# Performance work log

Hardware: AMD Instinct MI355X
Metric: run time of the kernel (lower is better)

## Reference

```python
import jax, jax.numpy as jnp
import numpy as np

N_NODES = 50000
N_EDGES = 800000
N_GRAPHS = 64
FEAT, EMB, HID, VOCAB = 128, 256, 512, 512


def setup_inputs() -> dict:
    key = jax.random.key(0)
    ks = jax.random.split(key, 16)
    def w(k, shape, fan_in):
        return jax.random.normal(k, shape, jnp.float32) / np.sqrt(fan_in)
    return {
        "prev_symbol": jax.random.randint(ks[0], (N_GRAPHS,), 0, VOCAB, jnp.int32),
        "x": jax.random.normal(ks[1], (N_NODES, FEAT), jnp.float32),
        "edge_index": jax.random.randint(ks[2], (2, N_EDGES), 0, N_NODES, jnp.int64),
        "batch": jnp.sort(jax.random.randint(ks[3], (N_NODES,), 0, N_GRAPHS, jnp.int64)),
        "W_root1": w(ks[4], (FEAT, EMB), FEAT),
        "W_rel1": w(ks[5], (FEAT, EMB), FEAT),
        "b1": jnp.zeros((EMB,), jnp.float32),
        "W_root2": w(ks[6], (EMB, HID), EMB),
        "W_rel2": w(ks[7], (EMB, HID), EMB),
        "b2": jnp.zeros((HID,), jnp.float32),
        "Wh": w(ks[8], (HID, HID), HID),
        "bh": jnp.zeros((HID,), jnp.float32),
        "Wc": w(ks[9], (HID, HID), HID),
        "bc": jnp.zeros((HID,), jnp.float32),
        "Wout": w(ks[10], (HID, VOCAB), HID),
        "bout": jnp.zeros((VOCAB,), jnp.float32),
    }


def _rgcn(x, edge_index, W_root, W_rel, b):
    # single-relation RGCNConv: root transform + mean-aggregated neighbor messages
    src, dst = edge_index[0], edge_index[1]
    msg = x[src] @ W_rel                                   # [E, out]
    agg = jax.ops.segment_sum(msg, dst, num_segments=N_NODES)
    cnt = jax.ops.segment_sum(jnp.ones((src.shape[0],), x.dtype), dst,
                              num_segments=N_NODES)
    agg = agg / jnp.maximum(cnt, 1.0)[:, None]
    return x @ W_root + agg + b


def reference(prev_symbol, x, edge_index, batch,
              W_root1, W_rel1, b1, W_root2, W_rel2, b2,
              Wh, bh, Wc, bc, Wout, bout):
    h = jax.nn.relu(_rgcn(x, edge_index, W_root1, W_rel1, b1))
    h = jax.nn.relu(_rgcn(h, edge_index, W_root2, W_rel2, b2))
    # global_mean_pool over graph ids
    s = jax.ops.segment_sum(h, batch, num_segments=N_GRAPHS)
    n = jax.ops.segment_sum(jnp.ones((h.shape[0],), h.dtype), batch,
                            num_segments=N_GRAPHS)
    pooled = s / jnp.maximum(n, 1.0)[:, None]              # [G, HID]
    hidden = pooled @ Wh + bh
    cell = pooled @ Wc + bc
    logits = jax.nn.log_softmax(hidden @ Wout + bout, axis=1)
    return (logits, hidden, cell)
```

## Files before the change

### kernel.cpp

```cpp
#include <hip/hip_runtime.h>
#include <hip/hip_bf16.h>

#define N_NODES 50000
#define N_EDGES 800000
#define N_GRAPHS 64
#define FEAT 128
#define EMB 256
#define HID 512
#define VOCAB 512

#define RB ((N_NODES + 127) / 128)
#define RPX ((RB + 7) / 8)
#define BKT 64

#define NPB 98
#define BCAP 10240
#define PA_EDGES 4096
#define PA_BLOCKS ((N_EDGES + PA_EDGES - 1) / PA_EDGES)
#define BC_STR 16

#define KC 4
#define KCH (HID / KC)
#define KO 4
#define KOH (HID / KO)

#define CONV_ELEMS (N_NODES * 32 + 256 * 256 + 512 * 512)
#define CONV_BLOCKS (CONV_ELEMS / 256)

typedef __attribute__((ext_vector_type(4))) float floatx4;
typedef __attribute__((ext_vector_type(2))) float floatx2;
typedef unsigned int uint32;
typedef unsigned char uchar_t;

__device__ __forceinline__ void accf8(uint32 u, float* a) {
    floatx2 lo = __builtin_amdgcn_cvt_pk_f32_fp8(u, false);
    floatx2 hi = __builtin_amdgcn_cvt_pk_f32_fp8(u, true);
    a[0] += lo[0]; a[1] += lo[1]; a[2] += hi[0]; a[3] += hi[1];
}
__device__ __forceinline__ uchar_t f2f8(float v) {
    return (uchar_t)(__builtin_amdgcn_cvt_pk_fp8_f32(v, v, 0, false) & 0xff);
}
__device__ __forceinline__ uint32 pk4f8(float a, float b, float c, float d) {
    uint32 w = __builtin_amdgcn_cvt_pk_fp8_f32(a, b, 0, false);
    return __builtin_amdgcn_cvt_pk_fp8_f32(c, d, w, true);
}
__device__ __forceinline__ void async16(const void* g, void* l) {
    __builtin_amdgcn_global_load_lds(
        (const __attribute__((address_space(1))) void*)g,
        (__attribute__((address_space(3))) void*)l, 16, 0, 0);
}

__global__ void prep_kernel(const int* __restrict__ edge, int* __restrict__ bktcnt,
                            int2* __restrict__ bktbuf,
                            const float* __restrict__ x,
                            const float* __restrict__ W01, const float* __restrict__ W11,
                            const float* __restrict__ W02, const float* __restrict__ W12,
                            uchar_t* __restrict__ xa8,
                            uchar_t* __restrict__ w1t8, uchar_t* __restrict__ w2t8) {
    if (blockIdx.x < PA_BLOCKS) {
        __shared__ int hist[NPB];
        __shared__ int excl[NPB];
        __shared__ int lpos[NPB];
        __shared__ int gbase[NPB];
        __shared__ int2 stage[PA_EDGES];
        const int t = threadIdx.x;
        const int e0 = blockIdx.x * PA_EDGES;
        const int ne = min(PA_EDGES, N_EDGES - e0);

        if (t < NPB) hist[t] = 0;
        __syncthreads();
        for (int s = t; s < ne; s += 256) {
            int d = edge[N_EDGES + e0 + s];
            atomicAdd(&hist[d >> 9], 1);
        }
        __syncthreads();
        if (t == 0) {
            int run = 0;
            for (int i = 0; i < NPB; ++i) { excl[i] = run; run += hist[i]; }
        }
        __syncthreads();
        if (t < NPB) {
            gbase[t] = atomicAdd(bktcnt + t * BC_STR, hist[t]);
            lpos[t] = excl[t];
        }
        __syncthreads();
        for (int s = t; s < ne; s += 256) {
            int src = edge[e0 + s];
            int d = edge[N_EDGES + e0 + s];
            int b = d >> 9;
            int lp = atomicAdd(&lpos[b], 1);
            stage[lp] = make_int2(src, d);
        }
        __syncthreads();
        for (int s = t; s < ne; s += 256) {
            int2 p = stage[s];
            int b = p.y >> 9;
            int g = gbase[b] + (s - excl[b]);
            if (g < BCAP) bktbuf[(size_t)b * BCAP + g] = p;
        }
    } else {
        int tid = (blockIdx.x - PA_BLOCKS) * 256 + threadIdx.x;
        if (tid < N_NODES * 32) {
            int row = tid >> 5, c = (tid & 31) * 4;
            float4 v = *(const float4*)(x + (size_t)row * FEAT + c);
            *(uint32*)(xa8 + (size_t)row * 256 + c) = pk4f8(v.x, v.y, v.z, v.w);
        } else if (tid < N_NODES * 32 + 256 * 256) {
            int t1 = tid - N_NODES * 32;
            int n = t1 >> 8, k = t1 & 255;
            float v = (k < 128) ? W01[(size_t)k * 256 + n] : W11[(size_t)(k - 128) * 256 + n];
            w1t8[t1] = f2f8(v);
        } else {
            int t2 = tid - N_NODES * 32 - 256 * 256;
            int n = t2 >> 9, k = t2 & 511;
            float v = (k < 256) ? W02[(size_t)k * 512 + n] : W12[(size_t)(k - 256) * 512 + n];
            w2t8[t2] = f2f8(v);
        }
    }
}

__global__ __launch_bounds__(256) void bucket_kernel(const int* __restrict__ bktcnt,
                                                     const int2* __restrict__ bktbuf,
                                                     int* __restrict__ srcbuf,
                                                     int* __restrict__ cnt) {
    __shared__ int lcur[512];
    const int b = blockIdx.x;
    const int t = threadIdx.x;
    const int n0 = b << 9;
    const int nn = min(512, N_NODES - n0);
    const int ne = min(bktcnt[b * BC_STR], BCAP);

    #pragma unroll
    for (int i = t; i < 512; i += 256) lcur[i] = 0;
    __syncthreads();
    for (int s = t; s < ne; s += 256) {
        int2 p = bktbuf[(size_t)b * BCAP + s];
        int d = p.y & 511;
        int k = atomicAdd(&lcur[d], 1);
        if (k < BKT) srcbuf[((size_t)(n0 + d) << 6) + k] = p.x;
    }
    __syncthreads();
    #pragma unroll
    for (int i = t; i < 512; i += 256)
        if (i < nn) cnt[n0 + i] = lcur[i];
}

__global__ __launch_bounds__(256) void gather1_kernel(
    const int* __restrict__ cnt, const int* __restrict__ srcbuf,
    uchar_t* __restrict__ xa8)
{
    int node = blockIdx.x * 4 + (threadIdx.x >> 6);
    if (node >= N_NODES) return;
    int lane = threadIdx.x & 63;
    int grp = lane >> 3;
    int l8 = lane & 7;
    int c_ = cnt[node];
    float ri = 1.0f / (float)max(c_, 1);
    int beg = node << 6;
    int end = beg + min(c_, BKT);

    float a[16];
    #pragma unroll
    for (int k = 0; k < 16; ++k) a[k] = 0.f;

    int j = beg + grp;
    for (; j + 8 < end; j += 16) {
        int s0 = srcbuf[j];
        int s1 = srcbuf[j + 8];
        uint4 u0 = *(const uint4*)(xa8 + (size_t)s0 * 256 + l8 * 16);
        uint4 u1 = *(const uint4*)(xa8 + (size_t)s1 * 256 + l8 * 16);
        accf8(u0.x, a + 0); accf8(u0.y, a + 4); accf8(u0.z, a + 8); accf8(u0.w, a + 12);
        accf8(u1.x, a + 0); accf8(u1.y, a + 4); accf8(u1.z, a + 8); accf8(u1.w, a + 12);
    }
    for (; j < end; j += 8) {
        int s0 = srcbuf[j];
        uint4 u0 = *(const uint4*)(xa8 + (size_t)s0 * 256 + l8 * 16);
        accf8(u0.x, a + 0); accf8(u0.y, a + 4); accf8(u0.z, a + 8); accf8(u0.w, a + 12);
    }
    #pragma unroll
    for (int k = 0; k < 16; ++k) a[k] += __shfl_down(a[k], 32);
    #pragma unroll
    for (int k = 0; k < 16; ++k) a[k] += __shfl_down(a[k], 16);
    #pragma unroll
    for (int k = 0; k < 16; ++k) a[k] += __shfl_down(a[k], 8);
    if (grp == 0) {
        uint4 o;
        o.x = pk4f8(a[0] * ri,  a[1] * ri,  a[2] * ri,  a[3] * ri);
        o.y = pk4f8(a[4] * ri,  a[5] * ri,  a[6] * ri,  a[7] * ri);
        o.z = pk4f8(a[8] * ri,  a[9] * ri,  a[10] * ri, a[11] * ri);
        o.w = pk4f8(a[12] * ri, a[13] * ri, a[14] * ri, a[15] * ri);
        *(uint4*)(xa8 + (size_t)node * 256 + 128 + l8 * 16) = o;
    }
}

__global__ __launch_bounds__(256) void gather2_kernel(
    const int* __restrict__ cnt, const int* __restrict__ srcbuf,
    uchar_t* __restrict__ h1a8)
{
    int node = blockIdx.x * 4 + (threadIdx.x >> 6);
    if (node >= N_NODES) return;
    int lane = threadIdx.x & 63;
    int grp = lane >> 4;
    int l16 = lane & 15;
    int c_ = cnt[node];
    float ri = 1.0f / (float)max(c_, 1);
    int beg = node << 6;
    int end = beg + min(c_, BKT);

    float a[16];
    #pragma unroll
    for (int k = 0; k < 16; ++k) a[k] = 0.f;

    int j = beg + grp;
    for (; j + 4 < end; j += 8) {
        int s0 = srcbuf[j];
        int s1 = srcbuf[j + 4];
        uint4 u0 = *(const uint4*)(h1a8 + (size_t)s0 * 512 + l16 * 16);
        uint4 u1 = *(const uint4*)(h1a8 + (size_t)s1 * 512 + l16 * 16);
        accf8(u0.x, a + 0); accf8(u0.y, a + 4); accf8(u0.z, a + 8); accf8(u0.w, a + 12);
        accf8(u1.x, a + 0); accf8(u1.y, a + 4); accf8(u1.z, a + 8); accf8(u1.w, a + 12);
    }
    for (; j < end; j += 4) {
        int s0 = srcbuf[j];
        uint4 u0 = *(const uint4*)(h1a8 + (size_t)s0 * 512 + l16 * 16);
        accf8(u0.x, a + 0); accf8(u0.y, a + 4); accf8(u0.z, a + 8); accf8(u0.w, a + 12);
    }
    #pragma unroll
    for (int k = 0; k < 16; ++k) a[k] += __shfl_down(a[k], 32);
    #pragma unroll
    for (int k = 0; k < 16; ++k) a[k] += __shfl_down(a[k], 16);
    if (grp == 0) {
        uint4 o;
        o.x = pk4f8(a[0] * ri,  a[1] * ri,  a[2] * ri,  a[3] * ri);
        o.y = pk4f8(a[4] * ri,  a[5] * ri,  a[6] * ri,  a[7] * ri);
        o.z = pk4f8(a[8] * ri,  a[9] * ri,  a[10] * ri, a[11] * ri);
        o.w = pk4f8(a[12] * ri, a[13] * ri, a[14] * ri, a[15] * ri);
        *(uint4*)(h1a8 + (size_t)node * 512 + 256 + l16 * 16) = o;
    }
}

template<int KTOT, int OUTSTR, bool POOL, int COLS>
__global__ __launch_bounds__(256) void mfma_gemm_f8(
    const uchar_t* __restrict__ A, const uchar_t* __restrict__ Bt,
    const float* __restrict__ bias, uchar_t* __restrict__ outf8,
    float* __restrict__ psum, const int* __restrict__ batch)
{
    __shared__ uchar_t As[16384];
    __shared__ uchar_t Bs[16384];
    __shared__ float pool2[8 * 128];

    const int id = blockIdx.x;
    const int xcd = id & 7;
    const int s_ = id >> 3;
    const int col = s_ & (COLS - 1);
    const int rloc = s_ / COLS;
    const int rowblk = xcd * RPX + rloc;
    if (rowblk >= RB) return;

    const int tid = threadIdx.x;
    const int lane = tid & 63;
    const int wave = tid >> 6;
    const int quad = lane >> 4;
    const int l16 = lane & 15;
    const int m0w = (wave & 1) * 64;
    const int n0w = (wave >> 1) * 64;
    const int row0 = rowblk * 128;
    const int col0 = col * 128;
    const int Mm1 = N_NODES - 1;

    int st_r[4], st_q[4];
    #pragma unroll
    for (int c = 0; c < 4; ++c) {
        int slot = c * 256 + tid;
        int r = slot >> 3;
        st_r[c] = r;
        st_q[c] = ((slot & 7) ^ (r & 7)) * 16;
    }

    floatx4 acc[4][4] = {};

    for (int kt = 0; kt < KTOT / 128; ++kt) {
        const int kb = kt * 128;
        #pragma unroll
        for (int c = 0; c < 4; ++c) {
            async16(A + (size_t)min(row0 + st_r[c], Mm1) * KTOT + kb + st_q[c],
                    &As[(c * 256 + wave * 64) * 16]);
        }
        #pragma unroll
        for (int c = 0; c < 4; ++c) {
            async16(Bt + (size_t)(col0 + st_r[c]) * KTOT + kb + st_q[c],
                    &Bs[(c * 256 + wave * 64) * 16]);
        }
        __syncthreads();
        #pragma unroll
        for (int kk = 0; kk < 4; ++kk) {
            const int c0 = kk * 2 + (quad >> 1);
            const int o8 = (quad & 1) * 8;
            long a[4], b[4];
            #pragma unroll
            for (int t = 0; t < 4; ++t) {
                int r = m0w + t * 16 + l16;
                a[t] = *(const long*)&As[r * 128 + ((c0 ^ (r & 7)) * 16) + o8];
            }
            #pragma unroll
            for (int t = 0; t < 4; ++t) {
                int r = n0w + t * 16 + l16;
                b[t] = *(const long*)&Bs[r * 128 + ((c0 ^ (r & 7)) * 16) + o8];
            }
            #pragma unroll
            for (int i = 0; i < 4; ++i)
                #pragma unroll
                for (int j = 0; j < 4; ++j)
                    acc[i][j] = __builtin_amdgcn_mfma_f32_16x16x32_fp8_fp8(a[i], b[j], acc[i][j], 0, 0, 0);
        }
        __syncthreads();
    }

    float bias4[4];
    #pragma unroll
    for (int j = 0; j < 4; ++j) bias4[j] = bias[col0 + n0w + j * 16 + l16];

    if (!POOL) {
        #pragma unroll
        for (int i = 0; i < 4; ++i) {
            #pragma unroll
            for (int r = 0; r < 4; ++r) {
                int m = row0 + m0w + i * 16 + quad * 4 + r;
                if (m < N_NODES) {
                    #pragma unroll
                    for (int j = 0; j < 4; ++j) {
                        float v = fmaxf(acc[i][j][r] + bias4[j], 0.f);
                        outf8[(size_t)m * OUTSTR + col0 + n0w + j * 16 + l16] = f2f8(v);
                    }
                }
            }
        }
    } else {
        int gmin = batch[row0];
        int gmax = batch[min(row0 + 127, N_NODES - 1)];
        int span = gmax - gmin + 1;
        if (span == 1) {
            float s[4] = {0.f, 0.f, 0.f, 0.f};
            #pragma unroll
            for (int i = 0; i < 4; ++i) {
                #pragma unroll
                for (int r = 0; r < 4; ++r) {
                    int m = row0 + m0w + i * 16 + quad * 4 + r;
                    if (m < N_NODES) {
                        #pragma unroll
                        for (int j = 0; j < 4; ++j)
                            s[j] += fmaxf(acc[i][j][r] + bias4[j], 0.f);
                    }
                }
            }
            int slot = (wave & 1) * 4 + quad;
            #pragma unroll
            for (int j = 0; j < 4; ++j)
                pool2[slot * 128 + n0w + j * 16 + l16] = s[j];
            __syncthreads();
            if (tid < 128) {
                float v = 0.f;
                #pragma unroll
                for (int k = 0; k < 8; ++k) v += pool2[k * 128 + tid];
                atomicAdd(psum + (size_t)gmin * HID + col0 + tid, v);
            }
        } else if (span <= 8) {
            for (int i = tid; i < span * 128; i += 256) pool2[i] = 0.f;
            __syncthreads();
            float s[4] = {0.f, 0.f, 0.f, 0.f};
            int cg = -1;
            #pragma unroll
            for (int i = 0; i < 4; ++i) {
                #pragma unroll
                for (int r = 0; r < 4; ++r) {
                    int m = row0 + m0w + i * 16 + quad * 4 + r;
                    if (m < N_NODES) {
                        int g = batch[m] - gmin;
                        if (g != cg) {
                            if (cg >= 0) {
                                #pragma unroll
                                for (int j = 0; j < 4; ++j)
                                    atomicAdd(&pool2[cg * 128 + n0w + j * 16 + l16], s[j]);
                            }
                            cg = g;
                            s[0] = s[1] = s[2] = s[3] = 0.f;
                        }
                        #pragma unroll
                        for (int j = 0; j < 4; ++j)
                            s[j] += fmaxf(acc[i][j][r] + bias4[j], 0.f);
                    }
                }
            }
            if (cg >= 0) {
                #pragma unroll
                for (int j = 0; j < 4; ++j)
                    atomicAdd(&pool2[cg * 128 + n0w + j * 16 + l16], s[j]);
            }
            __syncthreads();
            for (int i = tid; i < span * 128; i += 256) {
                float v = pool2[i];
                if (v != 0.f)
                    atomicAdd(psum + (size_t)(gmin + (i >> 7)) * HID + col0 + (i & 127), v);
            }
        } else {
            #pragma unroll
            for (int i = 0; i < 4; ++i) {
                #pragma unroll
                for (int r = 0; r < 4; ++r) {
                    int m = row0 + m0w + i * 16 + quad * 4 + r;
                    if (m < N_NODES) {
                        int g = batch[m];
                        #pragma unroll
                        for (int j = 0; j < 4; ++j) {
                            float v = fmaxf(acc[i][j][r] + bias4[j], 0.f);
                            atomicAdd(psum + (size_t)g * HID + col0 + n0w + j * 16 + l16, v);
                        }
                    }
                }
            }
        }
    }
}

__global__ __launch_bounds__(256) void head_hc_part(
    const float* __restrict__ psum, const float* __restrict__ Wh,
    const float* __restrict__ Wc, float* __restrict__ hpart,
    float* __restrict__ cpart)
{
    __shared__ float p[KCH];
    const int g = blockIdx.y, kc = blockIdx.z;
    const int k0 = kc * KCH;
    const int t = threadIdx.x;
    if (t < KCH) p[t] = psum[(size_t)g * HID + k0 + t];
    __syncthreads();
    const int tile = blockIdx.x * 4 + (t >> 6);
    const int col = tile * 64 + (t & 63);
    float h = 0.f, c = 0.f;
    #pragma unroll 8
    for (int k = 0; k < KCH; ++k) {
        float pk = p[k];
        h = fmaf(pk, Wh[(size_t)(k0 + k) * HID + col], h);
        c = fmaf(pk, Wc[(size_t)(k0 + k) * HID + col], c);
    }
    hpart[((size_t)kc * N_GRAPHS + g) * HID + col] = h;
    cpart[((size_t)kc * N_GRAPHS + g) * HID + col] = c;
}

__global__ __launch_bounds__(512) void head_out2_kernel(
    const float* __restrict__ hpart, const float* __restrict__ cpart,
    const int* __restrict__ batch,
    const float* __restrict__ bh, const float* __restrict__ bc,
    const float* __restrict__ Wout, float* __restrict__ lpart,
    float* __restrict__ out)
{
    __shared__ float hrow[HID];
    const int kc2 = blockIdx.x, g = blockIdx.y, j = threadIdx.x;

    int lo = 0, hi = N_NODES;
    while (lo < hi) { int mid = (lo + hi) >> 1; if (batch[mid] < g) lo = mid + 1; else hi = mid; }
    int lo2 = lo, hi2 = N_NODES;
    while (lo2 < hi2) { int mid = (lo2 + hi2) >> 1; if (batch[mid] < g + 1) lo2 = mid + 1; else hi2 = mid; }
    float inv = 1.0f / fmaxf((float)(lo2 - lo), 1.0f);

    float hs = 0.f, cs = 0.f;
    #pragma unroll
    for (int kc = 0; kc < KC; ++kc) {
        hs += hpart[((size_t)kc * N_GRAPHS + g) * HID + j];
        cs += cpart[((size_t)kc * N_GRAPHS + g) * HID + j];
    }
    float hv = fmaf(hs, inv, bh[j]);
    hrow[j] = hv;
    if (kc2 == 0) {
        out[(size_t)N_GRAPHS * VOCAB + (size_t)g * HID + j] = hv;
        out[(size_t)2 * N_GRAPHS * VOCAB + (size_t)g * HID + j] = fmaf(cs, inv, bc[j]);
    }
    __syncthreads();

    const int k0 = kc2 * KOH;
    float l = 0.f;
    #pragma unroll 8
    for (int k = 0; k < KOH; ++k)
        l = fmaf(hrow[k0 + k], Wout[(size_t)(k0 + k) * VOCAB + j], l);
    lpart[((size_t)kc2 * N_GRAPHS + g) * VOCAB + j] = l;
}

__global__ __launch_bounds__(512) void head_fin_kernel(
    const float* __restrict__ lpart, const float* __restrict__ bout,
    float* __restrict__ out)
{
    __shared__ float redm[8];
    __shared__ float reds[8];
    __shared__ float bm, bs;
    const int g = blockIdx.x, j = threadIdx.x;

    float l = bout[j];
    #pragma unroll
    for (int kc = 0; kc < KO; ++kc)
        l += lpart[((size_t)kc * N_GRAPHS + g) * VOCAB + j];

    const int lane = j & 63, wave = j >> 6;
    float m = l;
    #pragma unroll
    for (int o = 32; o > 0; o >>= 1) m = fmaxf(m, __shfl_down(m, o));
    if (lane == 0) redm[wave] = m;
    __syncthreads();
    if (j == 0) {
        float mm = redm[0];
        for (int w = 1; w < 8; ++w) mm = fmaxf(mm, redm[w]);
        bm = mm;
    }
    __syncthreads();
    m = bm;
    float e = __expf(l - m);
    float s = e;
    #pragma unroll
    for (int o = 32; o > 0; o >>= 1) s += __shfl_down(s, o);
    if (lane == 0) reds[wave] = s;
    __syncthreads();
    if (j == 0) {
        float ss = 0.f;
        for (int w = 0; w < 8; ++w) ss += reds[w];
        bs = ss;
    }
    __syncthreads();
    out[(size_t)g * VOCAB + j] = l - m - logf(bs);
}

extern "C" void kernel_launch(void* const* d_in, const int* in_sizes, int n_in,
                              void* d_out, int out_size, void* d_ws, size_t ws_size,
                              hipStream_t stream) {
    const float* x      = (const float*)d_in[1];
    const int*   edge   = (const int*)d_in[2];
    const int*   batch  = (const int*)d_in[3];
    const float* Wroot1 = (const float*)d_in[4];
    const float* Wrel1  = (const float*)d_in[5];
    const float* b1     = (const float*)d_in[6];
    const float* Wroot2 = (const float*)d_in[7];
    const float* Wrel2  = (const float*)d_in[8];
    const float* b2     = (const float*)d_in[9];
    const float* Wh     = (const float*)d_in[10];
    const float* bh     = (const float*)d_in[11];
    const float* Wc     = (const float*)d_in[12];
    const float* bc     = (const float*)d_in[13];
    const float* Wout   = (const float*)d_in[14];
    const float* bout   = (const float*)d_in[15];
    float* out = (float*)d_out;

    int*      bktcnt  = (int*)d_ws;
    float*    psum    = (float*)(bktcnt + 128 * BC_STR);
    int*      cnt     = (int*)(psum + N_GRAPHS * HID);
    int*      srcbuf  = cnt + N_NODES;
    int2*     bktbuf  = (int2*)(srcbuf + (size_t)N_NODES * BKT);
    uchar_t*  xa8     = (uchar_t*)(bktbuf + (size_t)NPB * BCAP);
    uchar_t*  w1t8    = xa8 + (size_t)N_NODES * 256;
    uchar_t*  h1a8    = w1t8 + 256 * 256;
    uchar_t*  w2t8    = h1a8 + (size_t)N_NODES * 512;
    float*    hpart   = (float*)(w2t8 + 512 * 512);
    float*    cpart   = hpart + (size_t)KC * N_GRAPHS * HID;
    float*    lpart   = cpart + (size_t)KC * N_GRAPHS * HID;

    hipMemsetAsync(d_ws, 0, (size_t)(128 * BC_STR + N_GRAPHS * HID) * 4, stream);

    prep_kernel<<<PA_BLOCKS + CONV_BLOCKS, 256, 0, stream>>>(
        edge, bktcnt, bktbuf, x, Wroot1, Wrel1, Wroot2, Wrel2, xa8, w1t8, w2t8);

    bucket_kernel<<<NPB, 256, 0, stream>>>(bktcnt, bktbuf, srcbuf, cnt);

    gather1_kernel<<<(N_NODES + 3) / 4, 256, 0, stream>>>(cnt, srcbuf, xa8);

    {
        mfma_gemm_f8<256, 512, false, 2><<<8 * RPX * 2, 256, 0, stream>>>(
            xa8, w1t8, b1, h1a8, nullptr, nullptr);
    }

    gather2_kernel<<<(N_NODES + 3) / 4, 256, 0, stream>>>(cnt, srcbuf, h1a8);

    {
        mfma_gemm_f8<512, 0, true, 4><<<8 * RPX * 4, 256, 0, stream>>>(
            h1a8, w2t8, b2, nullptr, psum, batch);
    }

    head_hc_part<<<dim3(2, 64, KC), 256, 0, stream>>>(psum, Wh, Wc, hpart, cpart);
    head_out2_kernel<<<dim3(KO, 64), 512, 0, stream>>>(
        hpart, cpart, batch, bh, bc, Wout, lpart, out);
    head_fin_kernel<<<N_GRAPHS, 512, 0, stream>>>(lpart, bout, out);
}
```

Baseline: 276.0 us.

## Double GEMM row tile to 256 to reuse B tiles; widen bucket kernel

Each FP8 MFMA GEMM block now computes two 128-row A tiles against one shared B tile, so B is staged in LDS once per 256 rows and half as many blocks are launched. Accumulators double to 2x4x4 floatx4 per wave, which raises register pressure and may lower occupancy. The pooling epilogue is looped per row subtile, with extra barriers between subtiles. Separately, the bucket kernel uses 512 threads so each thread handles one local counter slot.

Result: slower. 292.3 us (+5.9%).

```diff
diff --git a/kernel.cpp b/kernel.cpp
--- a/kernel.cpp
+++ b/kernel.cpp
@@ -9,9 +9,10 @@
 #define HID 512
 #define VOCAB 512
 
-#define RB ((N_NODES + 127) / 128)
-#define RPX ((RB + 7) / 8)
 #define BKT 64
+
+#define RB2 ((N_NODES + 255) / 256)
+#define RPX2 ((RB2 + 7) / 8)
 
 #define NPB 98
 #define BCAP 10240
@@ -118,7 +119,7 @@
     }
 }
 
-__global__ __launch_bounds__(256) void bucket_kernel(const int* __restrict__ bktcnt,
+__global__ __launch_bounds__(512) void bucket_kernel(const int* __restrict__ bktcnt,
                                                      const int2* __restrict__ bktbuf,
                                                      int* __restrict__ srcbuf,
                                                      int* __restrict__ cnt) {
@@ -129,19 +130,16 @@
     const int nn = min(512, N_NODES - n0);
     const int ne = min(bktcnt[b * BC_STR], BCAP);
 
-    #pragma unroll
-    for (int i = t; i < 512; i += 256) lcur[i] = 0;
-    __syncthreads();
-    for (int s = t; s < ne; s += 256) {
+    lcur[t] = 0;
+    __syncthreads();
+    for (int s = t; s < ne; s += 512) {
         int2 p = bktbuf[(size_t)b * BCAP + s];
         int d = p.y & 511;
         int k = atomicAdd(&lcur[d], 1);
         if (k < BKT) srcbuf[((size_t)(n0 + d) << 6) + k] = p.x;
     }
     __syncthreads();
-    #pragma unroll
-    for (int i = t; i < 512; i += 256)
-        if (i < nn) cnt[n0 + i] = lcur[i];
+    if (t < nn) cnt[n0 + t] = lcur[t];
 }
 
 __global__ __launch_bounds__(256) void gather1_kernel(
@@ -244,7 +242,7 @@
     const float* __restrict__ bias, uchar_t* __restrict__ outf8,
     float* __restrict__ psum, const int* __restrict__ batch)
 {
-    __shared__ uchar_t As[16384];
+    __shared__ uchar_t As[2][16384];
     __shared__ uchar_t Bs[16384];
     __shared__ float pool2[8 * 128];
 
@@ -253,8 +251,8 @@
     const int s_ = id >> 3;
     const int col = s_ & (COLS - 1);
     const int rloc = s_ / COLS;
-    const int rowblk = xcd * RPX + rloc;
-    if (rowblk >= RB) return;
+    const int rowblk = xcd * RPX2 + rloc;
+    if (rowblk >= RB2) return;
 
     const int tid = threadIdx.x;
     const int lane = tid & 63;
@@ -263,7 +261,7 @@
     const int l16 = lane & 15;
     const int m0w = (wave & 1) * 64;
     const int n0w = (wave >> 1) * 64;
-    const int row0 = rowblk * 128;
+    const int row0 = rowblk * 256;
     const int col0 = col * 128;
     const int Mm1 = N_NODES - 1;
 
@@ -276,14 +274,19 @@
         st_q[c] = ((slot & 7) ^ (r & 7)) * 16;
     }
 
-    floatx4 acc[4][4] = {};
+    floatx4 acc[2][4][4] = {};
 
     for (int kt = 0; kt < KTOT / 128; ++kt) {
         const int kb = kt * 128;
         #pragma unroll
         for (int c = 0; c < 4; ++c) {
             async16(A + (size_t)min(row0 + st_r[c], Mm1) * KTOT + kb + st_q[c],
-                    &As[(c * 256 + wave * 64) * 16]);
+                    &As[0][(c * 256 + wave * 64) * 16]);
+        }
+        #pragma unroll
+        for (int c = 0; c < 4; ++c) {
+            async16(A + (size_t)min(row0 + 128 + st_r[c], Mm1) * KTOT + kb + st_q[c],
+                    &As[1][(c * 256 + wave * 64) * 16]);
         }
         #pragma unroll
         for (int c = 0; c < 4; ++c) {
@@ -295,22 +298,26 @@
         for (int kk = 0; kk < 4; ++kk) {
             const int c0 = kk * 2 + (quad >> 1);
             const int o8 = (quad & 1) * 8;
-            long a[4], b[4];
-            #pragma unroll
-            for (int t = 0; t < 4; ++t) {
-                int r = m0w + t * 16 + l16;
-                a[t] = *(const long*)&As[r * 128 + ((c0 ^ (r & 7)) * 16) + o8];
-            }
+            long b[4];
             #pragma unroll
             for (int t = 0; t < 4; ++t) {
                 int r = n0w + t * 16 + l16;
                 b[t] = *(const long*)&Bs[r * 128 + ((c0 ^ (r & 7)) * 16) + o8];
             }
             #pragma unroll
-            for (int i = 0; i < 4; ++i)
-                #pragma unroll
-                for (int j = 0; j < 4; ++j)
-                    acc[i][j] = __builtin_amdgcn_mfma_f32_16x16x32_fp8_fp8(a[i], b[j], acc[i][j], 0, 0, 0);
+            for (int rt = 0; rt < 2; ++rt) {
+                long a[4];
+                #pragma unroll
+                for (int t = 0; t < 4; ++t) {
+                    int r = m0w + t * 16 + l16;
+                    a[t] = *(const long*)&As[rt][r * 128 + ((c0 ^ (r & 7)) * 16) + o8];
+                }
+                #pragma unroll
+                for (int i = 0; i < 4; ++i)
+                    #pragma unroll
+                    for (int j = 0; j < 4; ++j)
+                        acc[rt][i][j] = __builtin_amdgcn_mfma_f32_16x16x32_fp8_fp8(a[i], b[j], acc[rt][i][j], 0, 0, 0);
+            }
         }
         __syncthreads();
     }
@@ -319,100 +326,106 @@
     #pragma unroll
     for (int j = 0; j < 4; ++j) bias4[j] = bias[col0 + n0w + j * 16 + l16];
 
-    if (!POOL) {
-        #pragma unroll
-        for (int i = 0; i < 4; ++i) {
-            #pragma unroll
-            for (int r = 0; r < 4; ++r) {
-                int m = row0 + m0w + i * 16 + quad * 4 + r;
-                if (m < N_NODES) {
-                    #pragma unroll
-                    for (int j = 0; j < 4; ++j) {
-                        float v = fmaxf(acc[i][j][r] + bias4[j], 0.f);
-                        outf8[(size_t)m * OUTSTR + col0 + n0w + j * 16 + l16] = f2f8(v);
-                    }
-                }
-            }
-        }
-    } else {
-        int gmin = batch[row0];
-        int gmax = batch[min(row0 + 127, N_NODES - 1)];
-        int span = gmax - gmin + 1;
-        if (span == 1) {
-            float s[4] = {0.f, 0.f, 0.f, 0.f};
+    #pragma unroll
+    for (int rt = 0; rt < 2; ++rt) {
+        const int r0 = row0 + rt * 128;
+        if (!POOL) {
             #pragma unroll
             for (int i = 0; i < 4; ++i) {
                 #pragma unroll
                 for (int r = 0; r < 4; ++r) {
-                    int m = row0 + m0w + i * 16 + quad * 4 + r;
+                    int m = r0 + m0w + i * 16 + quad * 4 + r;
                     if (m < N_NODES) {
                         #pragma unroll
-                        for (int j = 0; j < 4; ++j)
-                            s[j] += fmaxf(acc[i][j][r] + bias4[j], 0.f);
+                        for (int j = 0; j < 4; ++j) {
+                            float v = fmaxf(acc[rt][i][j][r] + bias4[j], 0.f);
+                            outf8[(size_t)m * OUTSTR + col0 + n0w + j * 16 + l16] = f2f8(v);
+                        }
                     }
                 }
-            }
-            int slot = (wave & 1) * 4 + quad;
-            #pragma unroll
-            for (int j = 0; j < 4; ++j)
-                pool2[slot * 128 + n0w + j * 16 + l16] = s[j];
-            __syncthreads();
-            if (tid < 128) {
-                float v = 0.f;
-                #pragma unroll
-                for (int k = 0; k < 8; ++k) v += pool2[k * 128 + tid];
-                atomicAdd(psum + (size_t)gmin * HID + col0 + tid, v);
-            }
-        } else if (span <= 8) {
-            for (int i = tid; i < span * 128; i += 256) pool2[i] = 0.f;
-            __syncthreads();
-            float s[4] = {0.f, 0.f, 0.f, 0.f};
-            int cg = -1;
-            #pragma unroll
-            for (int i = 0; i < 4; ++i) {
-                #pragma unroll
-                for (int r = 0; r < 4; ++r) {
-                    int m = row0 + m0w + i * 16 + quad * 4 + r;
-                    if (m < N_NODES) {
-                        int g = batch[m] - gmin;
-                        if (g != cg) {
-                            if (cg >= 0) {
-                                #pragma unroll
-                                for (int j = 0; j < 4; ++j)
-                                    atomicAdd(&pool2[cg * 128 + n0w + j * 16 + l16], s[j]);
-                            }
-                            cg = g;
-                            s[0] = s[1] = s[2] = s[3] = 0.f;
-                        }
-                        #pragma unroll
-                        for (int j = 0; j < 4; ++j)
-                            s[j] += fmaxf(acc[i][j][r] + bias4[j], 0.f);
-                    }
-                }
-            }
-            if (cg >= 0) {
-                #pragma unroll
-                for (int j = 0; j < 4; ++j)
-                    atomicAdd(&pool2[cg * 128 + n0w + j * 16 + l16], s[j]);
-            }
-            __syncthreads();
-            for (int i = tid; i < span * 128; i += 256) {
-                float v = pool2[i];
-                if (v != 0.f)
-                    atomicAdd(psum + (size_t)(gmin + (i >> 7)) * HID + col0 + (i & 127), v);
             }
         } else {
-            #pragma unroll
-            for (int i = 0; i < 4; ++i) {
-                #pragma unroll
-                for (int r = 0; r < 4; ++r) {
-                    int m = row0 + m0w + i * 16 + quad * 4 + r;
-                    if (m < N_NODES) {
-                        int g = batch[m];
-                        #pragma unroll
-                        for (int j = 0; j < 4; ++j) {
-                            float v = fmaxf(acc[i][j][r] + bias4[j], 0.f);
-                            atomicAdd(psum + (size_t)g * HID + col0 + n0w + j * 16 + l16, v);
+            if (rt) __syncthreads();
+            if (r0 >= N_NODES) break;
+            int gmin = batch[r0];
+            int gmax = batch[min(r0 + 127, N_NODES - 1)];
+            int span = gmax - gmin + 1;
+            if (span == 1) {
+                float s[4] = {0.f, 0.f, 0.f, 0.f};
+                #pragma unroll
+                for (int i = 0; i < 4; ++i) {
+                    #pragma unroll
+                    for (int r = 0; r < 4; ++r) {
+                        int m = r0 + m0w + i * 16 + quad * 4 + r;
+                        if (m < N_NODES) {
+                            #pragma unroll
+                            for (int j = 0; j < 4; ++j)
+                                s[j] += fmaxf(acc[rt][i][j][r] + bias4[j], 0.f);
+                        }
+                    }
+                }
+                int slot = (wave & 1) * 4 + quad;
+                #pragma unroll
+                for (int j = 0; j < 4; ++j)
+                    pool2[slot * 128 + n0w + j * 16 + l16] = s[j];
+                __syncthreads();
+                if (tid < 128) {
+                    float v = 0.f;
+                    #pragma unroll
+                    for (int k = 0; k < 8; ++k) v += pool2[k * 128 + tid];
+                    atomicAdd(psum + (size_t)gmin * HID + col0 + tid, v);
+                }
+            } else if (span <= 8) {
+                for (int i = tid; i < span * 128; i += 256) pool2[i] = 0.f;
+                __syncthreads();
+                float s[4] = {0.f, 0.f, 0.f, 0.f};
+                int cg = -1;
+                #pragma unroll
+                for (int i = 0; i < 4; ++i) {
+                    #pragma unroll
+                    for (int r = 0; r < 4; ++r) {
+                        int m = r0 + m0w + i * 16 + quad * 4 + r;
+                        if (m < N_NODES) {
+                            int g = batch[m] - gmin;
+                            if (g != cg) {
+                                if (cg >= 0) {
+                                    #pragma unroll
+                                    for (int j = 0; j < 4; ++j)
+                                        atomicAdd(&pool2[cg * 128 + n0w + j * 16 + l16], s[j]);
+                                }
+                                cg = g;
+                                s[0] = s[1] = s[2] = s[3] = 0.f;
+                            }
+                            #pragma unroll
+                            for (int j = 0; j < 4; ++j)
+                                s[j] += fmaxf(acc[rt][i][j][r] + bias4[j], 0.f);
+                        }
+                    }
+                }
+                if (cg >= 0) {
+                    #pragma unroll
+                    for (int j = 0; j < 4; ++j)
+                        atomicAdd(&pool2[cg * 128 + n0w + j * 16 + l16], s[j]);
+                }
+                __syncthreads();
+                for (int i = tid; i < span * 128; i += 256) {
+                    float v = pool2[i];
+                    if (v != 0.f)
+                        atomicAdd(psum + (size_t)(gmin + (i >> 7)) * HID + col0 + (i & 127), v);
+                }
+            } else {
+                #pragma unroll
+                for (int i = 0; i < 4; ++i) {
+                    #pragma unroll
+                    for (int r = 0; r < 4; ++r) {
+                        int m = r0 + m0w + i * 16 + quad * 4 + r;
+                        if (m < N_NODES) {
+                            int g = batch[m];
+                            #pragma unroll
+                            for (int j = 0; j < 4; ++j) {
+                                float v = fmaxf(acc[rt][i][j][r] + bias4[j], 0.f);
+                                atomicAdd(psum + (size_t)g * HID + col0 + n0w + j * 16 + l16, v);
+                            }
                         }
                     }
                 }
@@ -563,19 +576,19 @@
     prep_kernel<<<PA_BLOCKS + CONV_BLOCKS, 256, 0, stream>>>(
         edge, bktcnt, bktbuf, x, Wroot1, Wrel1, Wroot2, Wrel2, xa8, w1t8, w2t8);
 
-    bucket_kernel<<<NPB, 256, 0, stream>>>(bktcnt, bktbuf, srcbuf, cnt);
+    bucket_kernel<<<NPB, 512, 0, stream>>>(bktcnt, bktbuf, srcbuf, cnt);
 
     gather1_kernel<<<(N_NODES + 3) / 4, 256, 0, stream>>>(cnt, srcbuf, xa8);
 
     {
-        mfma_gemm_f8<256, 512, false, 2><<<8 * RPX * 2, 256, 0, stream>>>(
+        mfma_gemm_f8<256, 512, false, 2><<<8 * RPX2 * 2, 256, 0, stream>>>(
             xa8, w1t8, b1, h1a8, nullptr, nullptr);
     }
 
     gather2_kernel<<<(N_NODES + 3) / 4, 256, 0, stream>>>(cnt, srcbuf, h1a8);
 
     {
-        mfma_gemm_f8<512, 0, true, 4><<<8 * RPX * 4, 256, 0, stream>>>(
+        mfma_gemm_f8<512, 0, true, 4><<<8 * RPX2 * 4, 256, 0, stream>>>(
             h1a8, w2t8, b2, nullptr, psum, batch);
     }
 
```
